# Kernel optimization log

Measured on AMD Instinct MI355X. Metric: run time of the kernel, lower is better.

Reference implementation:

```python
import jax, jax.numpy as jnp
import numpy as np

H, W = 480, 640  # image_sizeHW
L, N = 4096, 2048  # n_lines, points_per_line


def setup_inputs() -> dict:
    key = jax.random.key(0)
    k1, k2 = jax.random.split(key)
    # pixel coordinates in [0,W) x [0,H)
    input_tsr = jax.random.uniform(k1, (L, N, 2), dtype=jnp.float32) * jnp.array([W, H], jnp.float32)
    center = jnp.array([0.5, 0.5], jnp.float32)  # center pixel / [W, H]
    alpha = jnp.array(0.1, jnp.float32)
    return {"input_tsr": input_tsr, "center": center, "alpha": alpha}


def reference(input_tsr, center, alpha):
    # --- ScaleWithDimensions: x/W, y/H ---
    scaled = input_tsr / jnp.array([W, H], input_tsr.dtype)
    # --- Undistort (vectorized over all points) ---
    shifted = scaled - center                                  # [L,N,2]
    r2 = jnp.sum(shifted * shifted, axis=-1, keepdims=True)    # [L,N,1]
    und = (1.0 + alpha * r2) * shifted + center                # [L,N,2]
    # --- Line fit: min-eigenvector of A^T A, A = [x, y, -1] ---
    ones = jnp.ones(und.shape[:-1] + (1,), und.dtype)
    A = jnp.concatenate([und, -ones], axis=-1)                 # [L,N,3]
    M = jnp.einsum('lni,lnj->lij', A, A)                       # [L,3,3] symmetric PSD
    _, evecs = jnp.linalg.eigh(M)                              # ascending eigenvalues
    z = evecs[..., 0]                                          # [L,3] min-eigvec
    z = z / jnp.sqrt(z[:, 0] ** 2 + z[:, 1] ** 2)[:, None]
    theta = jnp.arctan2(z[:, 1], z[:, 0])                      # [L]
    rho = z[:, 2]                                              # [L]
    # original uses math.sin/torch.tensor(...) => line params are detached
    theta = jax.lax.stop_gradient(theta)
    rho = jax.lax.stop_gradient(rho)
    # --- Project each point onto its line; error = ||p' - p||^2 ---
    s = jnp.sin(theta)[:, None]
    c = jnp.cos(theta)[:, None]
    r = rho[:, None]
    x, y = und[..., 0], und[..., 1]
    b0 = x - r * c
    b1 = y - r * s
    beta = s * b0 - c * b1   # A is orthogonal: solve(A,b) = A^T b
    px = r * c + beta * s
    py = r * s - beta * c
    err = (px - x) ** 2 + (py - y) ** 2                        # [L,N]
    return jnp.sum(err, axis=1).astype(jnp.float32)            # [L]
```

## Files before the change

### kernel.cpp

```cpp
#include <hip/hip_runtime.h>
#include <math.h>

#define L_DIM 4096
#define N_DIM 2048
#define INV_W (1.0f / 640.0f)
#define INV_H (1.0f / 480.0f)
#define TWO_PI_3 2.0943951023931953

__global__ __launch_bounds__(256) void distopt_kernel(
    const float* __restrict__ inp,
    const float* __restrict__ center,
    const float* __restrict__ alpha_p,
    float* __restrict__ out)
{
    const int l = blockIdx.x;
    const int t = threadIdx.x;
    const float cx = center[0];
    const float cy = center[1];
    const float alpha = alpha_p[0];

    const float4* row = (const float4*)(inp + (size_t)l * (N_DIM * 2));

    float4 v[4];
#pragma unroll
    for (int i = 0; i < 4; ++i) v[i] = row[t + 256 * i];

    double sxx = 0.0, sxy = 0.0, syy = 0.0, sx = 0.0, sy = 0.0;
#pragma unroll
    for (int i = 0; i < 4; ++i) {
        float pxs[2] = { v[i].x, v[i].z };
        float pys[2] = { v[i].y, v[i].w };
#pragma unroll
        for (int j = 0; j < 2; ++j) {
            float shx = pxs[j] * INV_W - cx;
            float shy = pys[j] * INV_H - cy;
            float r2 = shx * shx + shy * shy;
            float f = 1.0f + alpha * r2;
            double ux = (double)(f * shx + cx);
            double uy = (double)(f * shy + cy);
            sxx += ux * ux;
            sxy += ux * uy;
            syy += uy * uy;
            sx  += ux;
            sy  += uy;
        }
    }

#pragma unroll
    for (int off = 32; off > 0; off >>= 1) {
        sxx += __shfl_down(sxx, off);
        sxy += __shfl_down(sxy, off);
        syy += __shfl_down(syy, off);
        sx  += __shfl_down(sx,  off);
        sy  += __shfl_down(sy,  off);
    }

    __shared__ double red[4][5];
    const int wave = t >> 6;
    if ((t & 63) == 0) {
        red[wave][0] = sxx; red[wave][1] = sxy; red[wave][2] = syy;
        red[wave][3] = sx;  red[wave][4] = sy;
    }
    __syncthreads();

    if (t == 0) {
        double Sxx = 0, Sxy = 0, Syy = 0, Sx = 0, Sy = 0;
#pragma unroll
        for (int w = 0; w < 4; ++w) {
            Sxx += red[w][0]; Sxy += red[w][1]; Syy += red[w][2];
            Sx  += red[w][3]; Sy  += red[w][4];
        }

        const double m00 = Sxx, m01 = Sxy, m02 = -Sx;
        const double m11 = Syy, m12 = -Sy;
        const double m22 = (double)N_DIM;

        double q  = (m00 + m11 + m22) * (1.0 / 3.0);
        double p1 = m01 * m01 + m02 * m02 + m12 * m12;
        double d0 = m00 - q, d1 = m11 - q, d2 = m22 - q;
        double p2 = d0 * d0 + d1 * d1 + d2 * d2 + 2.0 * p1;
        double p  = sqrt(p2 * (1.0 / 6.0));
        double ip = 1.0 / p;
        double b00 = d0 * ip, b11 = d1 * ip, b22 = d2 * ip;
        double b01 = m01 * ip, b02 = m02 * ip, b12 = m12 * ip;
        double detB = b00 * (b11 * b22 - b12 * b12)
                    - b01 * (b01 * b22 - b12 * b02)
                    + b02 * (b01 * b12 - b11 * b02);
        double r = detB * 0.5;
        r = fmin(1.0, fmax(-1.0, r));
        double phi = acos(r) * (1.0 / 3.0);
        double lam = q + 2.0 * p * cos(phi + TWO_PI_3);

        double a00 = m00 - lam, a11 = m11 - lam, a22 = m22 - lam;
        double c0x = m01 * m12 - m02 * a11;
        double c0y = m02 * m01 - a00 * m12;
        double c0z = a00 * a11 - m01 * m01;
        double c1x = m01 * a22 - m02 * m12;
        double c1y = m02 * m02 - a00 * a22;
        double c1z = a00 * m12 - m01 * m02;
        double c2x = a11 * a22 - m12 * m12;
        double c2y = m12 * m02 - m01 * a22;
        double c2z = m01 * m12 - a11 * m02;
        double n0 = c0x * c0x + c0y * c0y + c0z * c0z;
        double n1 = c1x * c1x + c1y * c1y + c1z * c1z;
        double n2 = c2x * c2x + c2y * c2y + c2z * c2z;

        double zx = c0x, zy = c0y, nn = n0;
        if (n1 > nn) { zx = c1x; zy = c1y; nn = n1; }
        if (n2 > nn) { zx = c2x; zy = c2y; nn = n2; }

        out[l] = (float)(lam * nn / (zx * zx + zy * zy));
    }
}

extern "C" void kernel_launch(void* const* d_in, const int* in_sizes, int n_in,
                              void* d_out, int out_size, void* d_ws, size_t ws_size,
                              hipStream_t stream) {
    const float* inp    = (const float*)d_in[0];
    const float* center = (const float*)d_in[1];
    const float* alpha  = (const float*)d_in[2];
    float* out = (float*)d_out;
    (void)in_sizes; (void)n_in; (void)d_ws; (void)ws_size;

    dim3 grid(out_size);
    dim3 block(256);
    hipLaunchKernelGGL(distopt_kernel, grid, block, 0, stream,
                       inp, center, alpha, out);
}
```

Measured before the change: 96.30 us.

## Assign one line per wavefront and drop block-level shared-memory reduction

Each 64-lane wavefront now processes one entire line, so a 256-thread block handles four lines and the grid shrinks by four. Each lane loads 16 float4 values instead of 4. The shared-memory reduction and __syncthreads are removed, and lane 0 of each wave solves the eigenproblem directly. This cuts block-level synchronisation and serial tail work. In exchange, each lane holds more registers and does longer serial fp64 accumulation, which may lower occupancy.

```diff
diff --git a/kernel.cpp b/kernel.cpp
--- a/kernel.cpp
+++ b/kernel.cpp
@@ -13,23 +13,26 @@
     const float* __restrict__ alpha_p,
     float* __restrict__ out)
 {
-    const int l = blockIdx.x;
-    const int t = threadIdx.x;
+    const int wave = threadIdx.x >> 6;
+    const int lane = threadIdx.x & 63;
+    const int l = blockIdx.x * 4 + wave;
+    if (l >= L_DIM) return;
+
     const float cx = center[0];
     const float cy = center[1];
     const float alpha = alpha_p[0];
 
     const float4* row = (const float4*)(inp + (size_t)l * (N_DIM * 2));
 
-    float4 v[4];
+    float4 v[16];
 #pragma unroll
-    for (int i = 0; i < 4; ++i) v[i] = row[t + 256 * i];
+    for (int k = 0; k < 16; ++k) v[k] = row[lane + 64 * k];
 
     double sxx = 0.0, sxy = 0.0, syy = 0.0, sx = 0.0, sy = 0.0;
 #pragma unroll
-    for (int i = 0; i < 4; ++i) {
-        float pxs[2] = { v[i].x, v[i].z };
-        float pys[2] = { v[i].y, v[i].w };
+    for (int k = 0; k < 16; ++k) {
+        float pxs[2] = { v[k].x, v[k].z };
+        float pys[2] = { v[k].y, v[k].w };
 #pragma unroll
         for (int j = 0; j < 2; ++j) {
             float shx = pxs[j] * INV_W - cx;
@@ -55,24 +58,9 @@
         sy  += __shfl_down(sy,  off);
     }
 
-    __shared__ double red[4][5];
-    const int wave = t >> 6;
-    if ((t & 63) == 0) {
-        red[wave][0] = sxx; red[wave][1] = sxy; red[wave][2] = syy;
-        red[wave][3] = sx;  red[wave][4] = sy;
-    }
-    __syncthreads();
-
-    if (t == 0) {
-        double Sxx = 0, Sxy = 0, Syy = 0, Sx = 0, Sy = 0;
-#pragma unroll
-        for (int w = 0; w < 4; ++w) {
-            Sxx += red[w][0]; Sxy += red[w][1]; Syy += red[w][2];
-            Sx  += red[w][3]; Sy  += red[w][4];
-        }
-
-        const double m00 = Sxx, m01 = Sxy, m02 = -Sx;
-        const double m11 = Syy, m12 = -Sy;
+    if (lane == 0) {
+        const double m00 = sxx, m01 = sxy, m02 = -sx;
+        const double m11 = syy, m12 = -sy;
         const double m22 = (double)N_DIM;
 
         double q  = (m00 + m11 + m22) * (1.0 / 3.0);
@@ -122,7 +110,7 @@
     float* out = (float*)d_out;
     (void)in_sizes; (void)n_in; (void)d_ws; (void)ws_size;
 
-    dim3 grid(out_size);
+    dim3 grid((out_size + 3) / 4);
     dim3 block(256);
     hipLaunchKernelGGL(distopt_kernel, grid, block, 0, stream,
                        inp, center, alpha, out);
```

After: 95.09 us. Within noise of the previous version (-1.3%).
